# Kernel optimization log

Measured on AMD Instinct MI355X. Metric: run time of the kernel, lower is better.

The kernel has to match this reference:

```python
import jax, jax.numpy as jnp
import numpy as np

N_NODES = 100000


def _gcn_conv(x, W, b, src, dst, n):
    # PyG GCNConv: h = x @ W; add self-loops; norm = d^-1/2[src] * d^-1/2[dst];
    # out[i] = sum_{(s->i)} norm * h[s] + b
    h = x @ W  # [N, F_out]
    deg = jax.ops.segment_sum(jnp.ones_like(dst, dtype=h.dtype), dst, num_segments=n)
    dis = jnp.where(deg > 0, jax.lax.rsqrt(jnp.maximum(deg, 1.0)), 0.0)
    norm = dis[src] * dis[dst]  # [E]
    msg = h[src] * norm[:, None]  # [E, F_out] gather + scale
    out = jax.ops.segment_sum(msg, dst, num_segments=n)  # scatter-add
    return out + b


def _add_self_loops(edge_index, n):
    loops = jnp.arange(n, dtype=edge_index.dtype)
    src = jnp.concatenate([edge_index[0], loops])
    dst = jnp.concatenate([edge_index[1], loops])
    return src, dst


def setup_inputs() -> dict:
    key = jax.random.key(0)
    k_x, k_e, k_w1, k_w2 = jax.random.split(key, 4)
    n, e, f_in, f_hid = N_NODES, 1600000, 128, 64
    x = jax.random.normal(k_x, (n, f_in), dtype=jnp.float32)
    edge_index = jax.random.randint(k_e, (2, e), 0, n, dtype=jnp.int64)
    # Glorot-ish init for weights
    W1 = jax.random.normal(k_w1, (f_in, f_hid), dtype=jnp.float32) / np.sqrt(f_in)
    b1 = jnp.zeros((f_hid,), dtype=jnp.float32)
    W2 = jax.random.normal(k_w2, (f_hid, f_hid), dtype=jnp.float32) / np.sqrt(f_hid)
    b2 = jnp.zeros((f_hid,), dtype=jnp.float32)
    return {"x": x, "edge_index": edge_index, "W1": W1, "b1": b1, "W2": W2, "b2": b2}


def reference(x, edge_index, W1, b1, W2, b2):
    n = x.shape[0]
    src, dst = _add_self_loops(edge_index, n)
    h = jax.nn.relu(_gcn_conv(x, W1, b1, src, dst, n))
    # F.dropout(training=False) in eval mode is identity
    out = _gcn_conv(h, W2, b2, src, dst, n)
    return out
```

## Files before the change

kernel.cpp:

```cpp
#include <hip/hip_runtime.h>
#include <hip/hip_bf16.h>


#define FOUT 64
#define BW 256
#define BSH 8
#define MAXB 512
#define CHUNK 4096
#define SLAB 6144

#define NT1 1024
#define NT2 512

__device__ __forceinline__ float bf2f(unsigned int u16) {
    union { unsigned int i; float f; } c;
    c.i = u16 << 16;
    return c.f;
}
__device__ __forceinline__ unsigned short f2bf(float f) {
    union { float f; unsigned int i; } c;
    c.f = f;
    unsigned int i = c.i;
    return (unsigned short)((i + 0x7FFFu + ((i >> 16) & 1u)) >> 16);
}

typedef __attribute__((ext_vector_type(8))) short short8v;
typedef __attribute__((ext_vector_type(4))) float f32x4;

__device__ __forceinline__ void split_frag(const float* xa, short8v* Ah, short8v* Al) {
    union { unsigned int u[4]; short8v v; } H, L;
#pragma unroll
    for (int p = 0; p < 4; p++) {
        unsigned short h0 = f2bf(xa[2 * p]);
        unsigned short h1 = f2bf(xa[2 * p + 1]);
        H.u[p] = (unsigned int)h0 | ((unsigned int)h1 << 16);
        unsigned short l0 = f2bf(xa[2 * p] - bf2f(h0));
        unsigned short l1 = f2bf(xa[2 * p + 1] - bf2f(h1));
        L.u[p] = (unsigned int)l0 | ((unsigned int)l1 << 16);
    }
    *Ah = H.v;
    *Al = L.v;
}

__device__ __forceinline__ void conv_w_frag(const float* __restrict__ W,
                                            unsigned short* __restrict__ WhF,
                                            unsigned short* __restrict__ WlF,
                                            int task) {
    const int lane = task & 63;
    const int cf = (task >> 6) & 3;
    const int s = task >> 8;
    const int q = lane >> 4, m = lane & 15;
#pragma unroll
    for (int j = 0; j < 8; j++) {
        int k = s * 32 + q * 8 + j;
        float x = W[(size_t)k * 64 + cf * 16 + m];
        unsigned short h = f2bf(x);
        WhF[(size_t)task * 8 + j] = h;
        WlF[(size_t)task * 8 + j] = f2bf(x - bf2f(h));
    }
}

__global__ __launch_bounds__(512) void edge_hist(
    const int* __restrict__ dst, int* __restrict__ cnt, int E,
    const float* __restrict__ W1, const float* __restrict__ W2,
    unsigned short* __restrict__ whf1, unsigned short* __restrict__ wlf1,
    unsigned short* __restrict__ whf2, unsigned short* __restrict__ wlf2) {
    __shared__ int h[MAXB];
    const int blk = blockIdx.x, t = threadIdx.x;
    h[t] = 0;
    __syncthreads();
    const int e0 = blk * CHUNK;
#pragma unroll
    for (int k = 0; k < CHUNK / 512; k++) {
        int e = e0 + k * 512 + t;
        if (e < E) atomicAdd(&h[dst[e] >> BSH], 1);
    }
    if (blk == 0) {
        for (int task = t; task < NT1 + NT2; task += 512) {
            if (task < NT1) conv_w_frag(W1, whf1, wlf1, task);
            else            conv_w_frag(W2, whf2, wlf2, task - NT1);
        }
    }
    __syncthreads();
    cnt[blk * MAXB + t] = h[t];
}

__global__ __launch_bounds__(512) void col_scan(int* __restrict__ cnt, int nblk,
                                                int* __restrict__ gcnt) {
    __shared__ int ts[512];
    const int b = blockIdx.x;
    const int t = threadIdx.x;
    int v = (t < nblk) ? cnt[t * MAXB + b] : 0;
    ts[t] = v;
    __syncthreads();
    for (int off = 1; off < 512; off <<= 1) {
        int x = (t >= off) ? ts[t - off] : 0;
        __syncthreads();
        ts[t] += x;
        __syncthreads();
    }
    if (t < nblk) cnt[t * MAXB + b] = b * SLAB + ts[t] - v;
    if (t == 511) gcnt[b] = ts[511];
}

__global__ __launch_bounds__(512) void edge_place(
    const int* __restrict__ src, const int* __restrict__ dst,
    const int* __restrict__ cnt, int* __restrict__ ebuf, int E) {
    __shared__ int lbase[MAXB];
    __shared__ int cur[MAXB];
    const int blk = blockIdx.x, t = threadIdx.x;
    lbase[t] = cnt[blk * MAXB + t];
    cur[t] = 0;
    __syncthreads();
    const int e0 = blk * CHUNK;
#pragma unroll
    for (int k = 0; k < CHUNK / 512; k++) {
        int e = e0 + k * 512 + t;
        if (e < E) {
            int d = dst[e];
            int b = d >> BSH;
            int r = atomicAdd(&cur[b], 1);
            ebuf[lbase[b] + r] = src[e] | ((d & (BW - 1)) << 17);
        }
    }
}

template <int K>
__global__ __launch_bounds__(512) void csr_gemm(
    int* __restrict__ ebuf, const int* __restrict__ gcnt,
    unsigned int* __restrict__ rowinfo, float* __restrict__ dis, int n,
    const float* __restrict__ X, const unsigned short* __restrict__ WhF,
    const unsigned short* __restrict__ WlF, unsigned short* __restrict__ HS) {
    __shared__ int ldeg[BW];
    __shared__ int lscan[BW];
    __shared__ float sdis[BW];
    const int b = blockIdx.x, t = threadIdx.x;
    const int node0 = b << BSH;
    const int nn = min(BW, n - node0);
    const int ebeg = b * SLAB;
    const int cnt = gcnt[b];

    int w[SLAB / 512];
#pragma unroll
    for (int k = 0; k < SLAB / 512; k++) {
        int idx = t + k * 512;
        w[k] = (idx < cnt) ? ebuf[ebeg + idx] : -1;
    }
    if (t < BW) ldeg[t] = 0;
    __syncthreads();
#pragma unroll
    for (int k = 0; k < SLAB / 512; k++)
        if (w[k] >= 0) atomicAdd(&ldeg[w[k] >> 17], 1);
    __syncthreads();
    int v = 0;
    if (t < BW) {
        v = ldeg[t];
        lscan[t] = v;
    }
    __syncthreads();
    for (int off = 1; off < BW; off <<= 1) {
        int x = 0;
        if (t < BW && t >= off) x = lscan[t - off];
        __syncthreads();
        if (t < BW) lscan[t] += x;
        __syncthreads();
    }
    if (t < nn) {
        int ex = lscan[t] - v;
        rowinfo[node0 + t] = ((unsigned int)(ebeg + ex) << 8) | (unsigned int)v;
        float dv = rsqrtf((float)v + 1.0f);
        dis[node0 + t] = dv;
        sdis[t] = dv;
    } else if (t < BW) {
        sdis[t] = 0.f;
    }
    __syncthreads();
    if (t < BW) ldeg[t] = lscan[t] - v;
    __syncthreads();
#pragma unroll
    for (int k = 0; k < SLAB / 512; k++)
        if (w[k] >= 0) {
            int r = atomicAdd(&ldeg[w[k] >> 17], 1);
            ebuf[ebeg + r] = w[k] & 0x1FFFF;
        }

    const int lane = t & 63;
    const int wvv = t >> 6;
    const int m = lane & 15;
    const int q = lane >> 4;
#pragma unroll 1
    for (int t2 = 0; t2 < 2; t2++) {
        const int tile = wvv * 2 + t2;
        const int wrow0 = node0 + tile * 16;
        f32x4 acc[4];
#pragma unroll
        for (int cf = 0; cf < 4; cf++) acc[cf] = (f32x4)0.f;

        const int arow = wrow0 + m;
        const bool rok = (arow < n);
        const float* xp = X + (size_t)arow * K + q * 8;
#pragma unroll
        for (int s = 0; s < K / 32; s++) {
            float4 v0, v1;
            if (rok) {
                v0 = *(const float4*)(xp + s * 32);
                v1 = *(const float4*)(xp + s * 32 + 4);
            } else {
                v0 = make_float4(0.f, 0.f, 0.f, 0.f);
                v1 = v0;
            }
            const float xa[8] = {v0.x, v0.y, v0.z, v0.w, v1.x, v1.y, v1.z, v1.w};
            short8v Ah, Al;
            split_frag(xa, &Ah, &Al);
            const unsigned short* wh = WhF + ((size_t)(s * 4) * 64 + lane) * 8;
            const unsigned short* wl = WlF + ((size_t)(s * 4) * 64 + lane) * 8;
#pragma unroll
            for (int cf = 0; cf < 4; cf++) {
                short8v bh = *(const short8v*)(wh + (size_t)cf * 64 * 8);
                short8v bl = *(const short8v*)(wl + (size_t)cf * 64 * 8);
                acc[cf] = __builtin_amdgcn_mfma_f32_16x16x32_bf16(Ah, bh, acc[cf], 0, 0, 0);
                acc[cf] = __builtin_amdgcn_mfma_f32_16x16x32_bf16(Al, bh, acc[cf], 0, 0, 0);
                acc[cf] = __builtin_amdgcn_mfma_f32_16x16x32_bf16(Ah, bl, acc[cf], 0, 0, 0);
            }
        }
#pragma unroll
        for (int r = 0; r < 4; r++) {
            int row = wrow0 + q * 4 + r;
            if (row < n) {
                float dr = sdis[tile * 16 + q * 4 + r];
#pragma unroll
                for (int cf = 0; cf < 4; cf++) {
                    HS[(size_t)row * FOUT + cf * 16 + m] = f2bf(acc[cf][r] * dr);
                }
            }
        }
    }
}

__device__ __forceinline__ void acc8(const uint4 u, float* a) {
    a[0] += bf2f(u.x & 0xFFFFu); a[1] += bf2f(u.x >> 16);
    a[2] += bf2f(u.y & 0xFFFFu); a[3] += bf2f(u.y >> 16);
    a[4] += bf2f(u.z & 0xFFFFu); a[5] += bf2f(u.z >> 16);
    a[6] += bf2f(u.w & 0xFFFFu); a[7] += bf2f(u.w >> 16);
}

#define OSTR 68
__global__ __launch_bounds__(256) void agg_gemm(
    const uint4* __restrict__ hsv, const unsigned int* __restrict__ rowinfo,
    const int* __restrict__ col, const float* __restrict__ dis,
    const float* __restrict__ bias,
    const unsigned short* __restrict__ WhF2, const unsigned short* __restrict__ WlF2,
    unsigned short* __restrict__ HS2, int n) {
    __shared__ float so[32 * OSTR];
    const int tid = threadIdx.x;
    const int wv = tid >> 6;
    const int lane = tid & 63;
    const int g = lane >> 3;
    const int jj = lane & 7;
    const int lrow = wv * 8 + g;
    const int i = blockIdx.x * 32 + lrow;

    float o[8];
#pragma unroll
    for (int p = 0; p < 8; p++) o[p] = 0.f;

    if (i < n) {
        const unsigned int info = rowinfo[i];
        const int beg = (int)(info >> 8);
        const int end = beg + (int)(info & 255u);

        float a[8];
        {
            uint4 su = hsv[(size_t)i * 8 + jj];
            a[0] = bf2f(su.x & 0xFFFFu); a[1] = bf2f(su.x >> 16);
            a[2] = bf2f(su.y & 0xFFFFu); a[3] = bf2f(su.y >> 16);
            a[4] = bf2f(su.z & 0xFFFFu); a[5] = bf2f(su.z >> 16);
            a[6] = bf2f(su.w & 0xFFFFu); a[7] = bf2f(su.w >> 16);
        }
        const int gb = g << 3;
        for (int chunk = beg; chunk < end; chunk += 8) {
            int m = end - chunk;
            if (m > 8) m = 8;
            int c = (chunk + jj < end) ? col[chunk + jj] : 0;
            int q = 0;
            for (; q + 4 <= m; q += 4) {
                int s0 = __shfl(c, gb + q);
                int s1 = __shfl(c, gb + q + 1);
                int s2 = __shfl(c, gb + q + 2);
                int s3 = __shfl(c, gb + q + 3);
                uint4 u0 = hsv[(size_t)s0 * 8 + jj];
                uint4 u1 = hsv[(size_t)s1 * 8 + jj];
                uint4 u2 = hsv[(size_t)s2 * 8 + jj];
                uint4 u3 = hsv[(size_t)s3 * 8 + jj];
                acc8(u0, a);
                acc8(u1, a);
                acc8(u2, a);
                acc8(u3, a);
            }
            for (; q < m; q++) {
                int s = __shfl(c, gb + q);
                acc8(hsv[(size_t)s * 8 + jj], a);
            }
        }
        float d = dis[i];
        const float4* b4 = (const float4*)bias;
        float4 bb0 = b4[jj * 2];
        float4 bb1 = b4[jj * 2 + 1];
        o[0] = fmaxf(d * a[0] + bb0.x, 0.f);
        o[1] = fmaxf(d * a[1] + bb0.y, 0.f);
        o[2] = fmaxf(d * a[2] + bb0.z, 0.f);
        o[3] = fmaxf(d * a[3] + bb0.w, 0.f);
        o[4] = fmaxf(d * a[4] + bb1.x, 0.f);
        o[5] = fmaxf(d * a[5] + bb1.y, 0.f);
        o[6] = fmaxf(d * a[6] + bb1.z, 0.f);
        o[7] = fmaxf(d * a[7] + bb1.w, 0.f);
    }
    {
        float* sp = &so[lrow * OSTR + jj * 8];
        *(float4*)sp = make_float4(o[0], o[1], o[2], o[3]);
        *(float4*)(sp + 4) = make_float4(o[4], o[5], o[6], o[7]);
    }
    __syncthreads();

    const int tile = wv >> 1;
    const int ch = wv & 1;
    const int m = lane & 15;
    const int q = lane >> 4;
    f32x4 acc[2];
    acc[0] = (f32x4)0.f;
    acc[1] = (f32x4)0.f;
#pragma unroll
    for (int s = 0; s < 2; s++) {
        const float* ap = &so[(tile * 16 + m) * OSTR + s * 32 + q * 8];
        float4 v0 = *(const float4*)ap;
        float4 v1 = *(const float4*)(ap + 4);
        const float xa[8] = {v0.x, v0.y, v0.z, v0.w, v1.x, v1.y, v1.z, v1.w};
        short8v Ah, Al;
        split_frag(xa, &Ah, &Al);
#pragma unroll
        for (int c = 0; c < 2; c++) {
            int cf = ch * 2 + c;
            const unsigned short* wh = WhF2 + ((size_t)(s * 4 + cf) * 64 + lane) * 8;
            const unsigned short* wl = WlF2 + ((size_t)(s * 4 + cf) * 64 + lane) * 8;
            short8v bh = *(const short8v*)wh;
            short8v bl = *(const short8v*)wl;
            acc[c] = __builtin_amdgcn_mfma_f32_16x16x32_bf16(Ah, bh, acc[c], 0, 0, 0);
            acc[c] = __builtin_amdgcn_mfma_f32_16x16x32_bf16(Al, bh, acc[c], 0, 0, 0);
            acc[c] = __builtin_amdgcn_mfma_f32_16x16x32_bf16(Ah, bl, acc[c], 0, 0, 0);
        }
    }
#pragma unroll
    for (int r = 0; r < 4; r++) {
        int lr = tile * 16 + q * 4 + r;
        int i2 = blockIdx.x * 32 + lr;
        if (i2 < n) {
            float dr = dis[i2];
#pragma unroll
            for (int c = 0; c < 2; c++) {
                HS2[(size_t)i2 * FOUT + (ch * 2 + c) * 16 + m] = f2bf(acc[c][r] * dr);
            }
        }
    }
}

template <bool RELU>
__global__ __launch_bounds__(256) void aggregate(
    const uint4* __restrict__ hsv, const unsigned int* __restrict__ rowinfo,
    const int* __restrict__ col, const float* __restrict__ dis,
    const float* __restrict__ bias, float* __restrict__ out, int n) {
    const int wave = blockIdx.x * 4 + (threadIdx.x >> 6);
    const int lane = threadIdx.x & 63;
    const int g  = lane >> 3;
    const int jj = lane & 7;
    const int i = wave * 8 + g;
    if (i >= n) return;

    const unsigned int info = rowinfo[i];
    const int beg = (int)(info >> 8);
    const int end = beg + (int)(info & 255u);

    float a[8];
    {
        uint4 su = hsv[(size_t)i * 8 + jj];
        a[0] = bf2f(su.x & 0xFFFFu); a[1] = bf2f(su.x >> 16);
        a[2] = bf2f(su.y & 0xFFFFu); a[3] = bf2f(su.y >> 16);
        a[4] = bf2f(su.z & 0xFFFFu); a[5] = bf2f(su.z >> 16);
        a[6] = bf2f(su.w & 0xFFFFu); a[7] = bf2f(su.w >> 16);
    }

    const int gb = g << 3;
    for (int chunk = beg; chunk < end; chunk += 8) {
        int m = end - chunk;
        if (m > 8) m = 8;
        int c = (chunk + jj < end) ? col[chunk + jj] : 0;
        int q = 0;
        for (; q + 4 <= m; q += 4) {
            int s0 = __shfl(c, gb + q);
            int s1 = __shfl(c, gb + q + 1);
            int s2 = __shfl(c, gb + q + 2);
            int s3 = __shfl(c, gb + q + 3);
            uint4 u0 = hsv[(size_t)s0 * 8 + jj];
            uint4 u1 = hsv[(size_t)s1 * 8 + jj];
            uint4 u2 = hsv[(size_t)s2 * 8 + jj];
            uint4 u3 = hsv[(size_t)s3 * 8 + jj];
            acc8(u0, a);
            acc8(u1, a);
            acc8(u2, a);
            acc8(u3, a);
        }
        for (; q < m; q++) {
            int s = __shfl(c, gb + q);
            acc8(hsv[(size_t)s * 8 + jj], a);
        }
    }
    float d = dis[i];
    const float4* b4 = (const float4*)bias;
    float4 bb0 = b4[jj * 2];
    float4 bb1 = b4[jj * 2 + 1];
    float4 o0, o1;
    o0.x = d * a[0] + bb0.x; o0.y = d * a[1] + bb0.y;
    o0.z = d * a[2] + bb0.z; o0.w = d * a[3] + bb0.w;
    o1.x = d * a[4] + bb1.x; o1.y = d * a[5] + bb1.y;
    o1.z = d * a[6] + bb1.z; o1.w = d * a[7] + bb1.w;
    if (RELU) {
        o0.x = fmaxf(o0.x, 0.f); o0.y = fmaxf(o0.y, 0.f);
        o0.z = fmaxf(o0.z, 0.f); o0.w = fmaxf(o0.w, 0.f);
        o1.x = fmaxf(o1.x, 0.f); o1.y = fmaxf(o1.y, 0.f);
        o1.z = fmaxf(o1.z, 0.f); o1.w = fmaxf(o1.w, 0.f);
    }
    float4* orow = (float4*)out + (size_t)i * 16 + jj * 2;
    orow[0] = o0;
    orow[1] = o1;
}

extern "C" void kernel_launch(void* const* d_in, const int* in_sizes, int n_in,
                              void* d_out, int out_size, void* d_ws, size_t ws_size,
                              hipStream_t stream) {
    const float* x  = (const float*)d_in[0];
    const int*   ei = (const int*)d_in[1];
    const float* W1 = (const float*)d_in[2];
    const float* b1 = (const float*)d_in[3];
    const float* W2 = (const float*)d_in[4];
    const float* b2 = (const float*)d_in[5];

    const int n = in_sizes[0] / 128;
    const int E = in_sizes[1] / 2;
    const int* srcp = ei;
    const int* dstp = ei + E;

    float* out = (float*)d_out;

    const int B = (n + BW - 1) / BW;
    const int nblk = (E + CHUNK - 1) / CHUNK;

    int*            cnt     = (int*)d_ws;
    int*            gcnt    = cnt + 512 * MAXB;
    unsigned int*   rowinfo = (unsigned int*)(gcnt + MAXB);
    float*          dis     = (float*)(rowinfo + n);
    int*            ebuf    = (int*)(dis + n);
    unsigned short* hs      = (unsigned short*)(ebuf + (size_t)B * SLAB);
    unsigned short* whf1    = hs + (size_t)n * FOUT;
    unsigned short* wlf1    = whf1 + (size_t)NT1 * 8;
    unsigned short* whf2    = wlf1 + (size_t)NT1 * 8;
    unsigned short* wlf2    = whf2 + (size_t)NT2 * 8;
    unsigned short* hs2     = wlf2 + (size_t)NT2 * 8;

    edge_hist<<<nblk, 512, 0, stream>>>(dstp, cnt, E, W1, W2,
                                        whf1, wlf1, whf2, wlf2);
    col_scan<<<B, 512, 0, stream>>>(cnt, nblk, gcnt);
    edge_place<<<nblk, 512, 0, stream>>>(srcp, dstp, cnt, ebuf, E);

    csr_gemm<128><<<B, 512, 0, stream>>>(ebuf, gcnt, rowinfo, dis, n,
                                         x, whf1, wlf1, hs);

    agg_gemm<<<(n + 31) / 32, 256, 0, stream>>>(
        (const uint4*)hs, rowinfo, ebuf, dis, b1, whf2, wlf2, hs2, n);

    aggregate<false><<<(n + 31) / 32, 256, 0, stream>>>(
        (const uint4*)hs2, rowinfo, ebuf, dis, b2, out, n);
}
```

Measured before the change: 224.0 us.

## Halve dst bucket width, shrink csr_gemm blocks, use wave-shuffle scan

Bucket width drops from 256 to 128 nodes, which doubles the bucket count to 1024 and halves the slab size. csr_gemm now runs 256-thread blocks with unconditional early loads of the slab. Its LDS Hillis-Steele scan, which needed many __syncthreads, is replaced by a wavefront shuffle scan plus a two-wave combine. The goal is more blocks, fewer barriers and better latency hiding in the CSR build. The cost is a larger histogram and col_scan work, and the GEMM tile mapping inside csr_gemm (previously 8 waves x 2 tiles of 16 rows) has to match the new 128-node, 4-wave layout.

```diff
diff --git a/kernel.cpp b/kernel.cpp
--- a/kernel.cpp
+++ b/kernel.cpp
@@ -3,11 +3,11 @@
 
 
 #define FOUT 64
-#define BW 256
-#define BSH 8
-#define MAXB 512
+#define BW 128
+#define BSH 7
+#define MAXB 1024
 #define CHUNK 4096
-#define SLAB 6144
+#define SLAB 3072
 
 #define NT1 1024
 #define NT2 512
@@ -68,6 +68,7 @@
     __shared__ int h[MAXB];
     const int blk = blockIdx.x, t = threadIdx.x;
     h[t] = 0;
+    h[t + 512] = 0;
     __syncthreads();
     const int e0 = blk * CHUNK;
 #pragma unroll
@@ -83,6 +84,7 @@
     }
     __syncthreads();
     cnt[blk * MAXB + t] = h[t];
+    cnt[blk * MAXB + t + 512] = h[t + 512];
 }
 
 __global__ __launch_bounds__(512) void col_scan(int* __restrict__ cnt, int nblk,
@@ -110,7 +112,9 @@
     __shared__ int cur[MAXB];
     const int blk = blockIdx.x, t = threadIdx.x;
     lbase[t] = cnt[blk * MAXB + t];
+    lbase[t + 512] = cnt[blk * MAXB + t + 512];
     cur[t] = 0;
+    cur[t + 512] = 0;
     __syncthreads();
     const int e0 = blk * CHUNK;
 #pragma unroll
@@ -126,47 +130,47 @@
 }
 
 template <int K>
-__global__ __launch_bounds__(512) void csr_gemm(
+__global__ __launch_bounds__(256) void csr_gemm(
     int* __restrict__ ebuf, const int* __restrict__ gcnt,
     unsigned int* __restrict__ rowinfo, float* __restrict__ dis, int n,
     const float* __restrict__ X, const unsigned short* __restrict__ WhF,
     const unsigned short* __restrict__ WlF, unsigned short* __restrict__ HS) {
     __shared__ int ldeg[BW];
-    __shared__ int lscan[BW];
     __shared__ float sdis[BW];
+    __shared__ int wtot[2];
     const int b = blockIdx.x, t = threadIdx.x;
     const int node0 = b << BSH;
     const int nn = min(BW, n - node0);
     const int ebeg = b * SLAB;
+
+    int raw[SLAB / 256];
+#pragma unroll
+    for (int k = 0; k < SLAB / 256; k++) raw[k] = ebuf[ebeg + t + k * 256];
+
     const int cnt = gcnt[b];
-
-    int w[SLAB / 512];
-#pragma unroll
-    for (int k = 0; k < SLAB / 512; k++) {
-        int idx = t + k * 512;
-        w[k] = (idx < cnt) ? ebuf[ebeg + idx] : -1;
-    }
     if (t < BW) ldeg[t] = 0;
     __syncthreads();
-#pragma unroll
-    for (int k = 0; k < SLAB / 512; k++)
+
+    int w[SLAB / 256];
+#pragma unroll
+    for (int k = 0; k < SLAB / 256; k++) {
+        w[k] = (t + k * 256 < cnt) ? raw[k] : -1;
         if (w[k] >= 0) atomicAdd(&ldeg[w[k] >> 17], 1);
-    __syncthreads();
-    int v = 0;
-    if (t < BW) {
-        v = ldeg[t];
-        lscan[t] = v;
-    }
-    __syncthreads();
-    for (int off = 1; off < BW; off <<= 1) {
-        int x = 0;
-        if (t < BW && t >= off) x = lscan[t - off];
-        __syncthreads();
-        if (t < BW) lscan[t] += x;
-        __syncthreads();
-    }
+    }
+    __syncthreads();
+
+    int v = 0, pv = 0;
+    if (t < BW) { v = ldeg[t]; pv = v; }
+#pragma unroll
+    for (int d = 1; d < 64; d <<= 1) {
+        int x = __shfl_up(pv, d);
+        if ((t & 63) >= d) pv += x;
+    }
+    if (t < BW && (t & 63) == 63) wtot[t >> 6] = pv;
+    __syncthreads();
+    if (t < BW && t >= 64) pv += wtot[0];
+    const int ex = pv - v;
     if (t < nn) {
-        int ex = lscan[t] - v;
         rowinfo[node0 + t] = ((unsigned int)(ebeg + ex) << 8) | (unsigned int)v;
         float dv = rsqrtf((float)v + 1.0f);
         dis[node0 + t] = dv;
@@ -174,11 +178,10 @@
     } else if (t < BW) {
         sdis[t] = 0.f;
     }
-    __syncthreads();
-    if (t < BW) ldeg[t] = lscan[t] - v;
-    __syncthreads();
-#pragma unroll
-    for (int k = 0; k < SLAB / 512; k++)
+    if (t < BW) ldeg[t] = ex;
+    __syncthreads();
+#pragma unroll
+    for (int k = 0; k < SLAB / 256; k++)
         if (w[k] >= 0) {
             int r = atomicAdd(&ldeg[w[k] >> 17], 1);
             ebuf[ebeg + r] = w[k] & 0x1FFFF;
@@ -470,7 +473,7 @@
     col_scan<<<B, 512, 0, stream>>>(cnt, nblk, gcnt);
     edge_place<<<nblk, 512, 0, stream>>>(srcp, dstp, cnt, ebuf, E);
 
-    csr_gemm<128><<<B, 512, 0, stream>>>(ebuf, gcnt, rowinfo, dis, n,
+    csr_gemm<128><<<B, 256, 0, stream>>>(ebuf, gcnt, rowinfo, dis, n,
                                          x, whf1, wlf1, hs);
 
     agg_gemm<<<(n + 31) / 32, 256, 0, stream>>>(
```

Result: no change. 224.3 us (+0.1%).
